# Performance work log

Hardware: AMD Instinct MI355X
Metric: run time of the kernel (lower is better)

Reference implementation:

```python
import jax, jax.numpy as jnp
import numpy as np

KSIZE = 3
KN = (KSIZE - 1) // 2  # 1
TEMP = 50.0


def _extract_patches(x, same_pad):
    """TF tf.image.extract_patches ordering: per location, (dy, dx, channel).
    x: [b,H,W,d] -> [b,h,w,9*d] (h=H,w=W if same_pad else H-2,W-2)."""
    if same_pad:
        x = jnp.pad(x, ((0, 0), (KN, KN), (KN, KN), (0, 0)))
    b, Hp, Wp, d = x.shape
    h, w = Hp - 2 * KN, Wp - 2 * KN
    slices = [x[:, dy:dy + h, dx:dx + w, :]
              for dy in range(KSIZE) for dx in range(KSIZE)]
    return jnp.concatenate(slices, axis=-1)


def setup_inputs() -> dict:
    key = jax.random.key(0)
    k1, k2, k3 = jax.random.split(key, 3)
    b, h, w, dims = 4, 48, 48, 64
    g_in = jax.random.normal(k1, (b, h, w, dims), dtype=jnp.float32)
    # binary inpainting mask (1 = known background, 0 = hole)
    mask = (jax.random.uniform(k2, (b, h, w, 1)) > 0.5).astype(jnp.float32)
    W2 = jax.random.normal(k3, (2 * dims, dims), dtype=jnp.float32) / np.sqrt(2.0 * dims)
    b2 = jnp.zeros((dims,), dtype=jnp.float32)
    return {"g_in": g_in, "mask": mask, "W2": W2, "b2": b2}


def reference(g_in, mask, W2, b2):
    b, h, w, dims = g_in.shape
    c = (h - 2 * KN) * (w - 2 * KN)

    mask_r = mask  # already (h,w,1); broadcasts over dims (== tile)
    bg = g_in * mask_r

    # p1: VALID 3x3 patches of bg -> dynamic kernels, [b, c, 9*dims]
    p1 = _extract_patches(bg, same_pad=False).reshape(b, c, KSIZE * KSIZE * dims)
    # p2: SAME 3x3 patches of g_in, [b, h, w, 9*dims]
    p2 = _extract_patches(g_in, same_pad=True)

    # cross-correlation: conv2d(ft, k1) == per-location dot with each bg patch
    CS = jnp.einsum('byxk,bjk->byxj', p2, p1)              # [b,h,w,c]
    k1d = jnp.sum(p1 * p1, axis=2)                          # [b,c]
    wwd = jnp.sum(p2 * p2, axis=3, keepdims=True)           # [b,h,w,1]
    DS1 = k1d[:, None, None, :] + wwd - 2.0 * CS            # squared distances
    mu = jnp.mean(DS1, axis=3, keepdims=True)
    sd = jnp.std(DS1, axis=3, keepdims=True)                # population std (tf.math.reduce_std)
    DS2 = -jnp.tanh((DS1 - mu) / sd)
    CA = jax.nn.softmax(TEMP * DS2, axis=-1)                # [b,h,w,c]

    # transposed conv aggregation with per-sample kernels k2[b,j,dy,dx,ch]
    k2 = p1.reshape(b, c, KSIZE, KSIZE, dims)
    CA_pad = jnp.pad(CA, ((0, 0), (KN, KN), (KN, KN), (0, 0)))
    acl = jnp.zeros((b, h, w, dims), dtype=g_in.dtype)
    for dy in range(KSIZE):
        for dx in range(KSIZE):
            win = CA_pad[:, 2 * KN - dy:2 * KN - dy + h, 2 * KN - dx:2 * KN - dx + w, :]
            acl = acl + jnp.einsum('byxj,bjd->byxd', win, k2[:, :, dy, dx, :])
    acl = acl / 9.0

    ACL = bg + acl * (1.0 - mask_r)
    con1 = jnp.concatenate([g_in, ACL], axis=3)             # [b,h,w,2*dims]
    return jax.nn.elu(jnp.einsum('byxk,kd->byxd', con1, W2) + b2)
```

## Files before the change

kernel.cpp:

```cpp
#include <hip/hip_runtime.h>
#include <hip/hip_fp16.h>
#include <math.h>

#define BB 4
#define HH 48
#define WW 48
#define DD 64
#define CH 46
#define CWp 46
#define CC (CH*CWp)
#define KK 576
#define HWp (HH*WW)
#define PW 50
#define PP (PW*PW)

#define SLOTW 48
#define NSLOT 2208
#define NGRP 276
#define QW 2304
#define QROWS 2500

typedef __attribute__((ext_vector_type(8))) short short8;
typedef __attribute__((ext_vector_type(8))) _Float16 half8;
typedef __attribute__((ext_vector_type(4))) float float4v;

#define OFFB_GPAD  ((size_t)0)
#define OFFB_BGPAD ((size_t)1280000)
#define OFFB_E     ((size_t)2560000)
#define OFFB_K1D   ((size_t)2596864)
#define OFFB_BGT   ((size_t)2632192)
#define OFFB_Q     ((size_t)3811840)
#define OFFB_S     ((size_t)49891840)
#define OFFB_W     ((size_t)90589696)
#define OFFB_ACL   ((size_t)133057024)

__device__ __forceinline__ ushort f2bf(float x) {
    unsigned u = __float_as_uint(x);
    return (ushort)((u + 0x7FFFu + ((u >> 16) & 1u)) >> 16);
}

__device__ __forceinline__ float waveReduceSum(float x) {
#pragma unroll
    for (int o = 32; o > 0; o >>= 1) x += __shfl_down(x, o, 64);
    return x;
}

__device__ __forceinline__ __half2 u2h2(uint u) {
    union { uint u; __half2 h; } c; c.u = u; return c.h;
}

__device__ __forceinline__ uint cvtpk_bf16(float lo, float hi) {
    uint r;
    asm("v_cvt_pk_bf16_f32 %0, %1, %2" : "=v"(r) : "v"(lo), "v"(hi));
    return r;
}

__device__ __forceinline__ float softexp(float d, float mu, float isd) {
    float z = (d - mu) * isd;
    float E2 = __expf(z + z);
    float r = __builtin_amdgcn_rcpf(E2 + 1.f);
    return __expf(fmaf(100.f, r, -50.f));
}

typedef __attribute__((address_space(3))) void lds_void_t;
typedef __attribute__((address_space(1))) void gmem_void_t;
__device__ __forceinline__ void gld16(const ushort* g, ushort* lds) {
    __builtin_amdgcn_global_load_lds((gmem_void_t*)g, (lds_void_t*)lds, 16, 0, 0);
}

__global__ __launch_bounds__(256) void build_pads(const float* __restrict__ g,
                                                  const float* __restrict__ mask,
                                                  ushort* __restrict__ gpad,
                                                  ushort* __restrict__ bgpad,
                                                  float* __restrict__ e) {
    int w = threadIdx.x >> 6, c = threadIdx.x & 63;
    int q4 = blockIdx.x * 4 + w;
    int b = q4 / PP, q = q4 % PP;
    int yp = q / PW, xp = q % PW;
    size_t o = (size_t)q4 * DD + c;
    if (yp >= 1 && yp <= HH && xp >= 1 && xp <= WW) {
        int pix = (yp - 1) * WW + (xp - 1);
        float gv = g[((size_t)b * HWp + pix) * DD + c];
        float m  = mask[(size_t)b * HWp + pix];
        float bgv = gv * m;
        gpad[o]  = f2bf(gv);
        bgpad[o] = f2bf(bgv);
        float ss = waveReduceSum(bgv * bgv);
        if (c == 0) e[b * HWp + pix] = ss;
    } else {
        gpad[o] = 0;
        bgpad[o] = 0;
    }
}

__global__ __launch_bounds__(256) void build_bgt_k1d(const ushort* __restrict__ bgpad,
                                                     const float* __restrict__ e,
                                                     ushort* __restrict__ bgT,
                                                     float* __restrict__ k1d) {
    int b = blockIdx.y;
    int t = threadIdx.x;
    if (blockIdx.x == 36) {
#pragma unroll 1
        for (int st = t; st < NSLOT; st += 256) {
            int jy = st / SLOTW, jx = st - jy * SLOTW;
            float s = 0.f;
            if (jx < CWp) {
                const float* eb = e + (size_t)b * HWp + jy * WW + jx;
#pragma unroll
                for (int ddy = 0; ddy < 3; ddy++)
#pragma unroll
                    for (int ddx = 0; ddx < 3; ddx++) s += eb[ddy * WW + ddx];
            }
            k1d[(size_t)b * NSLOT + st] = s;
        }
        return;
    }
    __shared__ ushort T[64 * 65];
    int jt = blockIdx.x;
    const ushort* src = bgpad + (size_t)b * PP * DD;
    int lr = t >> 3, c8 = (t & 7) * 8;
#pragma unroll
    for (int pass = 0; pass < 2; pass++) {
        int r = lr + pass * 32;
        int v = jt * 64 + r;
        int vy = v / 48, vx = v - vy * 48;
        uint4 d = *(const uint4*)(src + (size_t)((vy + 1) * PW + (vx + 1)) * DD + c8);
        ushort tmp[8];
        *(uint4*)tmp = d;
#pragma unroll
        for (int u = 0; u < 8; u++) {
            float f = __uint_as_float((uint)tmp[u] << 16);
            __half h = __float2half_rn(f);
            T[r * 65 + c8 + u] = *(ushort*)&h;
        }
    }
    __syncthreads();
#pragma unroll
    for (int pass = 0; pass < 2; pass++) {
        int c = lr + pass * 32;
        int j8 = (t & 7) * 8;
        ushort tmp[8];
#pragma unroll
        for (int u = 0; u < 8; u++) tmp[u] = T[(j8 + u) * 65 + c];
        *(uint4*)(bgT + ((size_t)b * 64 + c) * QW + jt * 64 + j8) = *(const uint4*)tmp;
    }
}

__global__ __launch_bounds__(256) void qgemm(const ushort* __restrict__ gpad,
                                             const ushort* __restrict__ bgpad,
                                             __half* __restrict__ Qout) {
    __shared__ ushort As[2 * 4096];
    __shared__ ushort Bs[2 * 4096];
    int i0 = blockIdx.x;
    int b = (i0 & 7) >> 1;
    int tile = ((i0 >> 3) << 1) | (i0 & 1);
    int ty = tile / 18, tx = tile - ty * 18;
    int m0 = ty * 128, n0 = tx * 128;
    const ushort* Ag = gpad + (size_t)b * PP * DD;
    const ushort* Bg = bgpad + (size_t)b * PP * DD;

    int tid = threadIdx.x;
    int l = tid & 63, w = tid >> 6;
    int quad = l >> 4, l15 = l & 15;
    int sw8 = (l15 >> 1) & 3;
    int wm = (w >> 1) * 64, wn = (w & 1) * 64;
    int rowInC = l >> 2;
    int cSw = (l & 3) ^ ((l >> 3) & 3);

#pragma unroll
    for (int i = 0; i < 2; i++) {
        int rg = w * 2 + i;
        int r = rg * 16 + rowInC;
        int u = m0 + r; if (u > QROWS - 1) u = QROWS - 1;
        int n = n0 + r;
        int vy = n / 48, vx = n - vy * 48;
        int baseA = u * DD + cSw * 8;
        int baseB = ((vy + 1) * PW + (vx + 1)) * DD + cSw * 8;
        gld16(Ag + baseA, As + rg * 512);
        gld16(Bg + baseB, Bs + rg * 512);
        gld16(Ag + baseA + 32, As + 4096 + rg * 512);
        gld16(Bg + baseB + 32, Bs + 4096 + rg * 512);
    }
    float4v acc[4][4];
#pragma unroll
    for (int i = 0; i < 4; i++)
#pragma unroll
        for (int j = 0; j < 4; j++) acc[i][j] = (float4v){0.f, 0.f, 0.f, 0.f};
    __syncthreads();
#pragma unroll
    for (int kb = 0; kb < 2; kb++) {
        const ushort* Ax = As + kb * 4096;
        const ushort* Bx = Bs + kb * 4096;
        short8 af[4], bf[4];
#pragma unroll
        for (int i = 0; i < 4; i++)
            af[i] = *(const short8*)&Ax[(wm + i * 16 + l15) * 32 + ((quad ^ sw8)) * 8];
#pragma unroll
        for (int j = 0; j < 4; j++)
            bf[j] = *(const short8*)&Bx[(wn + j * 16 + l15) * 32 + ((quad ^ sw8)) * 8];
#pragma unroll
        for (int i = 0; i < 4; i++)
#pragma unroll
            for (int j = 0; j < 4; j++)
                acc[i][j] = __builtin_amdgcn_mfma_f32_16x16x32_bf16(af[i], bf[j], acc[i][j], 0, 0, 0);
    }
    __half* C = Qout + (size_t)b * QROWS * QW;
#pragma unroll
    for (int i = 0; i < 4; i++) {
#pragma unroll
        for (int j = 0; j < 4; j++) {
            int n = n0 + wn + j * 16 + l15;
#pragma unroll
            for (int r = 0; r < 4; r++) {
                int m = m0 + wm + i * 16 + quad * 4 + r;
                if (m < QROWS) C[(size_t)m * QW + n] = __float2half(acc[i][j][r]);
            }
        }
    }
}

__global__ __launch_bounds__(320) void qrowsoft3(const __half* __restrict__ Q,
                                                 const float* __restrict__ k1d,
                                                 ushort* __restrict__ CA) {
    __shared__ float red[8][321];
    int i0 = blockIdx.x;
    int b = (i0 & 7) >> 1;
    int sub = ((i0 >> 3) << 1) | (i0 & 1);
    int y = sub / 12, xt = sub - y * 12;
    int x0 = xt * 4;

    int t = threadIdx.x;
    bool act = (t < NGRP);
    int jy = t / 6, jxb = (t - jy * 6) * 8;
    int slot0 = jy * SLOTW + jxb;
    bool vc6 = act && (jxb == 40);

    __half2 acc[4][4];
#pragma unroll
    for (int p = 0; p < 4; p++)
#pragma unroll
        for (int k = 0; k < 4; k++) acc[p][k] = u2h2(0u);

    float k1v[8] = {0.f, 0.f, 0.f, 0.f, 0.f, 0.f, 0.f, 0.f};

    if (act) {
        const float* k1 = k1d + (size_t)b * NSLOT + slot0;
        float4 ka = *(const float4*)k1;
        float4 kb = *(const float4*)(k1 + 4);
        k1v[0] = ka.x; k1v[1] = ka.y; k1v[2] = ka.z; k1v[3] = ka.w;
        k1v[4] = kb.x; k1v[5] = kb.y; k1v[6] = kb.z; k1v[7] = kb.w;

#pragma unroll 1
        for (int dy = 0; dy < 3; dy++) {
            const __half* rp = Q + ((size_t)b * QROWS + (size_t)(y + dy) * PW + x0) * QW
                               + slot0 + dy * 48;
            uint4 W4[6]; uint W1[6];
#pragma unroll
            for (int d = 0; d < 6; d++) {
                const __half* pr = rp + (size_t)d * QW;
                W4[d] = *(const uint4*)pr;
                W1[d] = *(const uint*)(pr + 8);
            }
#pragma unroll
            for (int d = 0; d < 6; d++) {
                uint w0 = W4[d].x, w1 = W4[d].y, w2 = W4[d].z, w3 = W4[d].w, w4 = W1[d];
                if (d < 4) {
                    acc[d][0] = __hadd2(acc[d][0], u2h2(w0));
                    acc[d][1] = __hadd2(acc[d][1], u2h2(w1));
                    acc[d][2] = __hadd2(acc[d][2], u2h2(w2));
                    acc[d][3] = __hadd2(acc[d][3], u2h2(w3));
                }
                if (d >= 1 && d <= 4) {
                    uint s0 = (w0 >> 16) | (w1 << 16);
                    uint s1 = (w1 >> 16) | (w2 << 16);
                    uint s2 = (w2 >> 16) | (w3 << 16);
                    uint s3 = (w3 >> 16) | (w4 << 16);
                    acc[d-1][0] = __hadd2(acc[d-1][0], u2h2(s0));
                    acc[d-1][1] = __hadd2(acc[d-1][1], u2h2(s1));
                    acc[d-1][2] = __hadd2(acc[d-1][2], u2h2(s2));
                    acc[d-1][3] = __hadd2(acc[d-1][3], u2h2(s3));
                }
                if (d >= 2) {
                    acc[d-2][0] = __hadd2(acc[d-2][0], u2h2(w1));
                    acc[d-2][1] = __hadd2(acc[d-2][1], u2h2(w2));
                    acc[d-2][2] = __hadd2(acc[d-2][2], u2h2(w3));
                    acc[d-2][3] = __hadd2(acc[d-2][3], u2h2(w4));
                }
            }
        }
    }

    if (vc6) {
#pragma unroll
        for (int p = 0; p < 4; p++) acc[p][3] = u2h2(0u);
    }

#pragma unroll
    for (int p = 0; p < 4; p++) {
        float s1p = 0.f, s2p = 0.f;
#pragma unroll
        for (int k = 0; k < 4; k++) {
            float2 f = __half22float2(acc[p][k]);
            float d0 = k1v[2*k]   - 2.f * f.x;
            float d1 = k1v[2*k+1] - 2.f * f.y;
            s1p += d0 + d1;
            s2p = fmaf(d0, d0, fmaf(d1, d1, s2p));
        }
        red[p][t] = s1p;
        red[4 + p][t] = s2p;
    }
    __syncthreads();
    if (t < 128) {
        int v = t >> 4, sb = t & 15;
        float s = 0.f;
#pragma unroll
        for (int k = 0; k < 20; k++) s += red[v][sb + 16 * k];
#pragma unroll
        for (int o = 8; o > 0; o >>= 1) s += __shfl_down(s, o, 16);
        if (sb == 0) red[v][320] = s;
    }
    __syncthreads();
    float mu[4], isd[4];
#pragma unroll
    for (int p = 0; p < 4; p++) {
        float m = red[p][320] * (1.f / (float)CC);
        float ex2 = red[4 + p][320] * (1.f / (float)CC);
        mu[p] = m;
        isd[p] = rsqrtf(ex2 - m * m);
    }

    uint eb[4][4];
#pragma unroll
    for (int p = 0; p < 4; p++) {
        float es = 0.f;
#pragma unroll
        for (int k = 0; k < 4; k++) {
            float2 f = __half22float2(acc[p][k]);
            float d0 = k1v[2*k]   - 2.f * f.x;
            float d1 = k1v[2*k+1] - 2.f * f.y;
            if (k == 3 && vc6) { d0 = 1e9f; d1 = 1e9f; }
            float e0 = softexp(d0, mu[p], isd[p]);
            float e1 = softexp(d1, mu[p], isd[p]);
            es += e0 + e1;
            eb[p][k] = cvtpk_bf16(e0, e1);
        }
        red[p][t] = act ? es : 0.f;
    }
    __syncthreads();
    if (t < 64) {
        int v = t >> 4, sb = t & 15;
        float s = 0.f;
#pragma unroll
        for (int k = 0; k < 20; k++) s += red[v][sb + 16 * k];
#pragma unroll
        for (int o = 8; o > 0; o >>= 1) s += __shfl_down(s, o, 16);
        if (sb == 0) red[v][320] = s;
    }
    __syncthreads();

    if (act) {
#pragma unroll
        for (int p = 0; p < 4; p++) {
            float iz = __builtin_amdgcn_rcpf(red[p][320]);
            uint o[4];
#pragma unroll
            for (int k = 0; k < 4; k++) {
                uint wv = eb[p][k];
                float lo = __uint_as_float(wv << 16) * iz;
                float hi = __uint_as_float(wv & 0xffff0000u) * iz;
                __half2 hh = __halves2half2(__float2half_rn(lo), __float2half_rn(hi));
                o[k] = *(uint*)&hh;
            }
            int pix = y * WW + x0 + p;
            ushort* wp = CA + ((size_t)b * HWp + pix) * (size_t)NSLOT + slot0;
            *(uint4*)wp = *(const uint4*)o;
        }
    }
}

__global__ __launch_bounds__(320) void boxsumW(const ushort* __restrict__ CAu,
                                               ushort* __restrict__ Wout) {
    int i0 = blockIdx.x;
    int b = (i0 & 7) >> 1;
    int sub = ((i0 >> 3) << 1) | (i0 & 1);
    int y = sub / 12, xt = sub - y * 12;
    int x0 = xt * 4;

    int t = threadIdx.x;
    if (t >= 288) return;
    int vy = t / 6, vx0 = (t - vy * 6) * 8;

    __half2 acc[4][4];
#pragma unroll
    for (int p = 0; p < 4; p++)
#pragma unroll
        for (int k = 0; k < 4; k++) acc[p][k] = u2h2(0u);

#pragma unroll
    for (int dy = 0; dy < 3; dy++) {
        int yy = y + 1 - dy;
        int jyv = vy - dy;
        if (yy < 0 || yy >= 48 || jyv < 0 || jyv >= 46) continue;
        const ushort* rp = CAu + (size_t)b * HWp * (size_t)NSLOT
                         + (ptrdiff_t)((yy * 48 + x0 - 1) * NSLOT + jyv * 48 + vx0 - 2);
        uint4 W4[6]; uint W1[6];
#pragma unroll
        for (int d = 0; d < 6; d++) {
            int xp = x0 - 1 + d;
            if (xp >= 0 && xp < 48) {
                W4[d] = *(const uint4*)(rp + (size_t)d * NSLOT);
                W1[d] = *(const uint*)(rp + (size_t)d * NSLOT + 8);
            } else {
                W4[d] = make_uint4(0u, 0u, 0u, 0u); W1[d] = 0u;
            }
        }
#pragma unroll
        for (int d = 0; d < 6; d++) {
            uint w0 = W4[d].x, w1 = W4[d].y, w2 = W4[d].z, w3 = W4[d].w, w4 = W1[d];
            if (vx0 == 0) w0 = 0u;
            if (d < 4) {
                acc[d][0] = __hadd2(acc[d][0], u2h2(w0));
                acc[d][1] = __hadd2(acc[d][1], u2h2(w1));
                acc[d][2] = __hadd2(acc[d][2], u2h2(w2));
                acc[d][3] = __hadd2(acc[d][3], u2h2(w3));
            }
            if (d >= 1 && d <= 4) {
                uint s0 = (w0 >> 16) | (w1 << 16);
                uint s1 = (w1 >> 16) | (w2 << 16);
                uint s2 = (w2 >> 16) | (w3 << 16);
                uint s3 = (w3 >> 16) | (w4 << 16);
                acc[d-1][0] = __hadd2(acc[d-1][0], u2h2(s0));
                acc[d-1][1] = __hadd2(acc[d-1][1], u2h2(s1));
                acc[d-1][2] = __hadd2(acc[d-1][2], u2h2(s2));
                acc[d-1][3] = __hadd2(acc[d-1][3], u2h2(s3));
            }
            if (d >= 2) {
                acc[d-2][0] = __hadd2(acc[d-2][0], u2h2(w1));
                acc[d-2][1] = __hadd2(acc[d-2][1], u2h2(w2));
                acc[d-2][2] = __hadd2(acc[d-2][2], u2h2(w3));
                acc[d-2][3] = __hadd2(acc[d-2][3], u2h2(w4));
            }
        }
    }

#pragma unroll
    for (int p = 0; p < 4; p++) {
        uint o[4];
#pragma unroll
        for (int k = 0; k < 4; k++) {
            __half2 h = acc[p][k];
            o[k] = *(uint*)&h;
        }
        size_t row = (size_t)b * HWp + (size_t)(y * 48 + x0 + p);
        *(uint4*)(Wout + row * QW + vy * 48 + vx0) = *(const uint4*)o;
    }
}

__global__ __launch_bounds__(256) void gemm3(const ushort* __restrict__ Wm,
                                             const ushort* __restrict__ bgT,
                                             float* __restrict__ aclp) {
    __shared__ ushort As[2 * 4096];
    __shared__ ushort Bs[2 * 2048];
    int i0 = blockIdx.x;
    int s = i0 & 7;
    int b = (i0 >> 3) & 3;
    int mt = i0 >> 5;
    int m0 = mt * 128;
    int kb = s * 288, ke = kb + 288;
    const ushort* Ab = Wm + ((size_t)b * HWp + m0) * QW;
    const ushort* Bb = bgT + (size_t)b * 64 * QW;

    int tid = threadIdx.x;
    int l = tid & 63, w = tid >> 6;
    int quad = l >> 4, l15 = l & 15;
    int sw8 = (l15 >> 1) & 3;
    int wm = w * 32;
    int rowInC = l >> 2;
    int cSw = (l & 3) ^ ((l >> 3) & 3);

    float4v acc[2][4];
#pragma unroll
    for (int i = 0; i < 2; i++)
#pragma unroll
        for (int j = 0; j < 4; j++) acc[i][j] = (float4v){0.f, 0.f, 0.f, 0.f};

#pragma unroll
    for (int i = 0; i < 2; i++) {
        int rg = w * 2 + i;
        gld16(Ab + (size_t)(rg * 16 + rowInC) * QW + kb + cSw * 8, As + rg * 512);
    }
    gld16(Bb + (size_t)(w * 16 + rowInC) * QW + kb + cSw * 8, Bs + w * 512);

    int buf = 0;
    for (int k0 = kb; k0 < ke; k0 += 32) {
        __syncthreads();
        int nb = buf ^ 1;
        if (k0 + 32 < ke) {
#pragma unroll
            for (int i = 0; i < 2; i++) {
                int rg = w * 2 + i;
                gld16(Ab + (size_t)(rg * 16 + rowInC) * QW + (k0 + 32) + cSw * 8,
                      As + nb * 4096 + rg * 512);
            }
            gld16(Bb + (size_t)(w * 16 + rowInC) * QW + (k0 + 32) + cSw * 8,
                  Bs + nb * 2048 + w * 512);
        }
        const ushort* Ax = As + buf * 4096;
        const ushort* Bx = Bs + buf * 2048;
        half8 af[2], bf[4];
#pragma unroll
        for (int i = 0; i < 2; i++)
            af[i] = *(const half8*)&Ax[(wm + i * 16 + l15) * 32 + ((quad ^ sw8)) * 8];
#pragma unroll
        for (int j = 0; j < 4; j++)
            bf[j] = *(const half8*)&Bx[(j * 16 + l15) * 32 + ((quad ^ sw8)) * 8];
#pragma unroll
        for (int i = 0; i < 2; i++)
#pragma unroll
            for (int j = 0; j < 4; j++)
                acc[i][j] = __builtin_amdgcn_mfma_f32_16x16x32_f16(af[i], bf[j], acc[i][j], 0, 0, 0);
        buf = nb;
    }

    float* C = aclp + ((size_t)s * (BB * HWp) + (size_t)b * HWp) * 64;
#pragma unroll
    for (int i = 0; i < 2; i++)
#pragma unroll
        for (int j = 0; j < 4; j++)
#pragma unroll
            for (int r = 0; r < 4; r++) {
                int m = m0 + wm + i * 16 + quad * 4 + r;
                int n = j * 16 + l15;
                C[(size_t)m * 64 + n] = acc[i][j][r];
            }
}

__global__ __launch_bounds__(256) void final_k2(const float* __restrict__ g,
                                                const float* __restrict__ mask,
                                                const float* __restrict__ aclp,
                                                const float* __restrict__ W2,
                                                const float* __restrict__ b2,
                                                float* __restrict__ out) {
    int w = threadIdx.x >> 6, d = threadIdx.x & 63;
    int pix = blockIdx.x * 4 + w;

    __shared__ float con1[4][128];
    float acl = 0.f;
    const float* ap = aclp + (size_t)pix * 64 + d;
#pragma unroll
    for (int s = 0; s < 8; s++) acl += ap[(size_t)s * (BB * HWp) * 64];

    float m = mask[pix];
    float gv = g[(size_t)pix * DD + d];
    float bgv = gv * m;
    float ACL = bgv + (acl / 9.f) * (1.f - m);
    con1[w][d] = gv;
    con1[w][64 + d] = ACL;
    __syncthreads();
    float accv = b2[d];
#pragma unroll 8
    for (int k = 0; k < 128; k++) accv = fmaf(con1[w][k], W2[k * 64 + d], accv);
    out[(size_t)pix * DD + d] = accv > 0.f ? accv : expm1f(accv);
}

extern "C" void kernel_launch(void* const* d_in, const int* in_sizes, int n_in,
                              void* d_out, int out_size, void* d_ws, size_t ws_size,
                              hipStream_t stream) {
    const float* g    = (const float*)d_in[0];
    const float* mask = (const float*)d_in[1];
    const float* W2   = (const float*)d_in[2];
    const float* b2   = (const float*)d_in[3];
    float* out = (float*)d_out;
    char* ws = (char*)d_ws;

    ushort* gpad  = (ushort*)(ws + OFFB_GPAD);
    ushort* bgpad = (ushort*)(ws + OFFB_BGPAD);
    float*  e     = (float*) (ws + OFFB_E);
    float*  k1d   = (float*) (ws + OFFB_K1D);
    ushort* bgT   = (ushort*)(ws + OFFB_BGT);
    __half* Qbuf  = (__half*)(ws + OFFB_Q);
    ushort* CA    = (ushort*)(ws + OFFB_S);
    ushort* Wbuf  = (ushort*)(ws + OFFB_W);
    float*  aclp  = (float*) (ws + OFFB_ACL);

    build_pads<<<BB * PP / 4, 256, 0, stream>>>(g, mask, gpad, bgpad, e);
    build_bgt_k1d<<<dim3(37, BB), 256, 0, stream>>>(bgpad, e, bgT, k1d);

    qgemm<<<1440, 256, 0, stream>>>(gpad, bgpad, Qbuf);
    qrowsoft3<<<BB * HWp / 4, 320, 0, stream>>>(Qbuf, k1d, CA);

    boxsumW<<<BB * HWp / 4, 320, 0, stream>>>(CA, Wbuf);
    gemm3<<<576, 256, 0, stream>>>(Wbuf, bgT, aclp);

    final_k2<<<BB * HWp / 4, 256, 0, stream>>>(g, mask, aclp, W2, b2, out);
}
```

Baseline: 167.7 us.

## Move dx shifts into GEMM K dimension, splitting box sums between GEMMs and epilogue

Measured after the change: 169.6 us. No clear change (+1.1%).

```diff
diff --git a/kernel.cpp b/kernel.cpp
--- a/kernel.cpp
+++ b/kernel.cpp
@@ -6,10 +6,7 @@
 #define HH 48
 #define WW 48
 #define DD 64
-#define CH 46
-#define CWp 46
-#define CC (CH*CWp)
-#define KK 576
+#define CC 2116
 #define HWp (HH*WW)
 #define PW 50
 #define PP (PW*PW)
@@ -17,6 +14,7 @@
 #define SLOTW 48
 #define NSLOT 2208
 #define NGRP 276
+#define KSPLIT0 1120
 #define QW 2304
 #define QROWS 2500
 
@@ -28,11 +26,11 @@
 #define OFFB_BGPAD ((size_t)1280000)
 #define OFFB_E     ((size_t)2560000)
 #define OFFB_K1D   ((size_t)2596864)
-#define OFFB_BGT   ((size_t)2632192)
-#define OFFB_Q     ((size_t)3811840)
-#define OFFB_S     ((size_t)49891840)
-#define OFFB_W     ((size_t)90589696)
-#define OFFB_ACL   ((size_t)133057024)
+#define OFFB_BGT3  ((size_t)2632192)
+#define OFFB_F     ((size_t)6023680)
+#define OFFB_CA    ((size_t)52103680)
+#define OFFB_CAY   ((size_t)92801536)
+#define OFFB_ACLP  ((size_t)133499392)
 
 __device__ __forceinline__ ushort f2bf(float x) {
     unsigned u = __float_as_uint(x);
@@ -93,18 +91,18 @@
     }
 }
 
-__global__ __launch_bounds__(256) void build_bgt_k1d(const ushort* __restrict__ bgpad,
-                                                     const float* __restrict__ e,
-                                                     ushort* __restrict__ bgT,
-                                                     float* __restrict__ k1d) {
+__global__ __launch_bounds__(256) void build_bgt3_k1d(const ushort* __restrict__ bgpad,
+                                                      const float* __restrict__ e,
+                                                      ushort* __restrict__ bgT3,
+                                                      float* __restrict__ k1d) {
     int b = blockIdx.y;
     int t = threadIdx.x;
-    if (blockIdx.x == 36) {
+    if (blockIdx.x == 35) {
 #pragma unroll 1
         for (int st = t; st < NSLOT; st += 256) {
             int jy = st / SLOTW, jx = st - jy * SLOTW;
             float s = 0.f;
-            if (jx < CWp) {
+            if (jx < 46) {
                 const float* eb = e + (size_t)b * HWp + jy * WW + jx;
 #pragma unroll
                 for (int ddy = 0; ddy < 3; ddy++)
@@ -115,7 +113,7 @@
         }
         return;
     }
-    __shared__ ushort T[64 * 65];
+    __shared__ ushort T[66 * 65];
     int jt = blockIdx.x;
     const ushort* src = bgpad + (size_t)b * PP * DD;
     int lr = t >> 3, c8 = (t & 7) * 8;
@@ -134,21 +132,43 @@
             T[r * 65 + c8 + u] = *(ushort*)&h;
         }
     }
+    if (t < 16) {
+        int r = 64 + (t >> 3);
+        int c8b = (t & 7) * 8;
+        int v = jt * 64 + r;
+        int vy = v / 48, vx = v - vy * 48;
+        uint4 d = *(const uint4*)(src + (size_t)((vy + 1) * PW + (vx + 1)) * DD + c8b);
+        ushort tmp[8];
+        *(uint4*)tmp = d;
+#pragma unroll
+        for (int u = 0; u < 8; u++) {
+            float f = __uint_as_float((uint)tmp[u] << 16);
+            __half h = __float2half_rn(f);
+            T[r * 65 + c8b + u] = *(ushort*)&h;
+        }
+    }
     __syncthreads();
 #pragma unroll
     for (int pass = 0; pass < 2; pass++) {
         int c = lr + pass * 32;
         int j8 = (t & 7) * 8;
-        ushort tmp[8];
-#pragma unroll
-        for (int u = 0; u < 8; u++) tmp[u] = T[(j8 + u) * 65 + c];
-        *(uint4*)(bgT + ((size_t)b * 64 + c) * QW + jt * 64 + j8) = *(const uint4*)tmp;
-    }
-}
-
-__global__ __launch_bounds__(256) void qgemm(const ushort* __restrict__ gpad,
+        int col0 = jt * 64 + j8;
+        if (col0 < NSLOT) {
+#pragma unroll
+            for (int dx = 0; dx < 3; dx++) {
+                ushort tmp[8];
+#pragma unroll
+                for (int u = 0; u < 8; u++) tmp[u] = T[(j8 + u + dx) * 65 + c];
+                *(uint4*)(bgT3 + ((size_t)b * 192 + dx * 64 + c) * NSLOT + col0) =
+                    *(const uint4*)tmp;
+            }
+        }
+    }
+}
+
+__global__ __launch_bounds__(256) void fgemm(const ushort* __restrict__ gpad,
                                              const ushort* __restrict__ bgpad,
-                                             __half* __restrict__ Qout) {
+                                             __half* __restrict__ Fout) {
     __shared__ ushort As[2 * 4096];
     __shared__ ushort Bs[2 * 4096];
     int i0 = blockIdx.x;
@@ -167,6 +187,7 @@
     int rowInC = l >> 2;
     int cSw = (l & 3) ^ ((l >> 3) & 3);
 
+    int baseA[2], baseB[2];
 #pragma unroll
     for (int i = 0; i < 2; i++) {
         int rg = w * 2 + i;
@@ -174,23 +195,37 @@
         int u = m0 + r; if (u > QROWS - 1) u = QROWS - 1;
         int n = n0 + r;
         int vy = n / 48, vx = n - vy * 48;
-        int baseA = u * DD + cSw * 8;
-        int baseB = ((vy + 1) * PW + (vx + 1)) * DD + cSw * 8;
-        gld16(Ag + baseA, As + rg * 512);
-        gld16(Bg + baseB, Bs + rg * 512);
-        gld16(Ag + baseA + 32, As + 4096 + rg * 512);
-        gld16(Bg + baseB + 32, Bs + 4096 + rg * 512);
-    }
+        baseA[i] = u * DD + cSw * 8;
+        baseB[i] = ((vy + 1) * PW + (vx + 1)) * DD + cSw * 8;
+    }
+
     float4v acc[4][4];
 #pragma unroll
     for (int i = 0; i < 4; i++)
 #pragma unroll
         for (int j = 0; j < 4; j++) acc[i][j] = (float4v){0.f, 0.f, 0.f, 0.f};
-    __syncthreads();
-#pragma unroll
-    for (int kb = 0; kb < 2; kb++) {
-        const ushort* Ax = As + kb * 4096;
-        const ushort* Bx = Bs + kb * 4096;
+
+#pragma unroll
+    for (int i = 0; i < 2; i++) {
+        int rg = w * 2 + i;
+        gld16(Ag + baseA[i], As + rg * 512);
+        gld16(Bg + baseB[i], Bs + rg * 512);
+    }
+
+    int buf = 0;
+    for (int k0 = 0; k0 < 192; k0 += 32) {
+        __syncthreads();
+        int nb = buf ^ 1;
+        if (k0 + 32 < 192) {
+#pragma unroll
+            for (int i = 0; i < 2; i++) {
+                int rg = w * 2 + i;
+                gld16(Ag + baseA[i] + (k0 + 32), As + nb * 4096 + rg * 512);
+                gld16(Bg + baseB[i] + (k0 + 32), Bs + nb * 4096 + rg * 512);
+            }
+        }
+        const ushort* Ax = As + buf * 4096;
+        const ushort* Bx = Bs + buf * 4096;
         short8 af[4], bf[4];
 #pragma unroll
         for (int i = 0; i < 4; i++)
@@ -203,8 +238,10 @@
 #pragma unroll
             for (int j = 0; j < 4; j++)
                 acc[i][j] = __builtin_amdgcn_mfma_f32_16x16x32_bf16(af[i], bf[j], acc[i][j], 0, 0, 0);
-    }
-    __half* C = Qout + (size_t)b * QROWS * QW;
+        buf = nb;
+    }
+
+    __half* C = Fout + (size_t)b * QROWS * QW;
 #pragma unroll
     for (int i = 0; i < 4; i++) {
 #pragma unroll
@@ -219,7 +256,7 @@
     }
 }
 
-__global__ __launch_bounds__(320) void qrowsoft3(const __half* __restrict__ Q,
+__global__ __launch_bounds__(320) void qrowsoft4(const __half* __restrict__ F,
                                                  const float* __restrict__ k1d,
                                                  ushort* __restrict__ CA) {
     __shared__ float red[8][321];
@@ -250,42 +287,17 @@
         k1v[0] = ka.x; k1v[1] = ka.y; k1v[2] = ka.z; k1v[3] = ka.w;
         k1v[4] = kb.x; k1v[5] = kb.y; k1v[6] = kb.z; k1v[7] = kb.w;
 
-#pragma unroll 1
+#pragma unroll
         for (int dy = 0; dy < 3; dy++) {
-            const __half* rp = Q + ((size_t)b * QROWS + (size_t)(y + dy) * PW + x0) * QW
-                               + slot0 + dy * 48;
-            uint4 W4[6]; uint W1[6];
-#pragma unroll
-            for (int d = 0; d < 6; d++) {
-                const __half* pr = rp + (size_t)d * QW;
-                W4[d] = *(const uint4*)pr;
-                W1[d] = *(const uint*)(pr + 8);
-            }
-#pragma unroll
-            for (int d = 0; d < 6; d++) {
-                uint w0 = W4[d].x, w1 = W4[d].y, w2 = W4[d].z, w3 = W4[d].w, w4 = W1[d];
-                if (d < 4) {
-                    acc[d][0] = __hadd2(acc[d][0], u2h2(w0));
-                    acc[d][1] = __hadd2(acc[d][1], u2h2(w1));
-                    acc[d][2] = __hadd2(acc[d][2], u2h2(w2));
-                    acc[d][3] = __hadd2(acc[d][3], u2h2(w3));
-                }
-                if (d >= 1 && d <= 4) {
-                    uint s0 = (w0 >> 16) | (w1 << 16);
-                    uint s1 = (w1 >> 16) | (w2 << 16);
-                    uint s2 = (w2 >> 16) | (w3 << 16);
-                    uint s3 = (w3 >> 16) | (w4 << 16);
-                    acc[d-1][0] = __hadd2(acc[d-1][0], u2h2(s0));
-                    acc[d-1][1] = __hadd2(acc[d-1][1], u2h2(s1));
-                    acc[d-1][2] = __hadd2(acc[d-1][2], u2h2(s2));
-                    acc[d-1][3] = __hadd2(acc[d-1][3], u2h2(s3));
-                }
-                if (d >= 2) {
-                    acc[d-2][0] = __hadd2(acc[d-2][0], u2h2(w1));
-                    acc[d-2][1] = __hadd2(acc[d-2][1], u2h2(w2));
-                    acc[d-2][2] = __hadd2(acc[d-2][2], u2h2(w3));
-                    acc[d-2][3] = __hadd2(acc[d-2][3], u2h2(w4));
-                }
+            const __half* R = F + ((size_t)b * QROWS + (size_t)(y + dy) * PW + x0) * QW
+                            + slot0 + dy * 48;
+#pragma unroll
+            for (int p = 0; p < 4; p++) {
+                uint4 v4 = *(const uint4*)(R + (size_t)p * QW);
+                acc[p][0] = __hadd2(acc[p][0], u2h2(v4.x));
+                acc[p][1] = __hadd2(acc[p][1], u2h2(v4.y));
+                acc[p][2] = __hadd2(acc[p][2], u2h2(v4.z));
+                acc[p][3] = __hadd2(acc[p][3], u2h2(v4.w));
             }
         }
     }
@@ -378,8 +390,8 @@
     }
 }
 
-__global__ __launch_bounds__(320) void boxsumW(const ushort* __restrict__ CAu,
-                                               ushort* __restrict__ Wout) {
+__global__ __launch_bounds__(320) void cay_k(const ushort* __restrict__ CAu,
+                                             ushort* __restrict__ CAy) {
     int i0 = blockIdx.x;
     int b = (i0 & 7) >> 1;
     int sub = ((i0 >> 3) << 1) | (i0 & 1);
@@ -387,8 +399,9 @@
     int x0 = xt * 4;
 
     int t = threadIdx.x;
-    if (t >= 288) return;
-    int vy = t / 6, vx0 = (t - vy * 6) * 8;
+    if (t >= NGRP) return;
+    int jy = t / 6, jxb = (t - jy * 6) * 8;
+    int slot0 = jy * SLOTW + jxb;
 
     __half2 acc[4][4];
 #pragma unroll
@@ -399,47 +412,17 @@
 #pragma unroll
     for (int dy = 0; dy < 3; dy++) {
         int yy = y + 1 - dy;
-        int jyv = vy - dy;
-        if (yy < 0 || yy >= 48 || jyv < 0 || jyv >= 46) continue;
-        const ushort* rp = CAu + (size_t)b * HWp * (size_t)NSLOT
-                         + (ptrdiff_t)((yy * 48 + x0 - 1) * NSLOT + jyv * 48 + vx0 - 2);
-        uint4 W4[6]; uint W1[6];
-#pragma unroll
-        for (int d = 0; d < 6; d++) {
-            int xp = x0 - 1 + d;
-            if (xp >= 0 && xp < 48) {
-                W4[d] = *(const uint4*)(rp + (size_t)d * NSLOT);
-                W1[d] = *(const uint*)(rp + (size_t)d * NSLOT + 8);
-            } else {
-                W4[d] = make_uint4(0u, 0u, 0u, 0u); W1[d] = 0u;
-            }
-        }
-#pragma unroll
-        for (int d = 0; d < 6; d++) {
-            uint w0 = W4[d].x, w1 = W4[d].y, w2 = W4[d].z, w3 = W4[d].w, w4 = W1[d];
-            if (vx0 == 0) w0 = 0u;
-            if (d < 4) {
-                acc[d][0] = __hadd2(acc[d][0], u2h2(w0));
-                acc[d][1] = __hadd2(acc[d][1], u2h2(w1));
-                acc[d][2] = __hadd2(acc[d][2], u2h2(w2));
-                acc[d][3] = __hadd2(acc[d][3], u2h2(w3));
-            }
-            if (d >= 1 && d <= 4) {
-                uint s0 = (w0 >> 16) | (w1 << 16);
-                uint s1 = (w1 >> 16) | (w2 << 16);
-                uint s2 = (w2 >> 16) | (w3 << 16);
-                uint s3 = (w3 >> 16) | (w4 << 16);
-                acc[d-1][0] = __hadd2(acc[d-1][0], u2h2(s0));
-                acc[d-1][1] = __hadd2(acc[d-1][1], u2h2(s1));
-                acc[d-1][2] = __hadd2(acc[d-1][2], u2h2(s2));
-                acc[d-1][3] = __hadd2(acc[d-1][3], u2h2(s3));
-            }
-            if (d >= 2) {
-                acc[d-2][0] = __hadd2(acc[d-2][0], u2h2(w1));
-                acc[d-2][1] = __hadd2(acc[d-2][1], u2h2(w2));
-                acc[d-2][2] = __hadd2(acc[d-2][2], u2h2(w3));
-                acc[d-2][3] = __hadd2(acc[d-2][3], u2h2(w4));
-            }
+        if (yy < 0 || yy >= 48) continue;
+        if (jy < dy) continue;
+        const ushort* rp = CAu + ((size_t)b * HWp + yy * 48 + x0) * (size_t)NSLOT
+                         + slot0 - 48 * dy;
+#pragma unroll
+        for (int p = 0; p < 4; p++) {
+            uint4 v4 = *(const uint4*)(rp + (size_t)p * NSLOT);
+            acc[p][0] = __hadd2(acc[p][0], u2h2(v4.x));
+            acc[p][1] = __hadd2(acc[p][1], u2h2(v4.y));
+            acc[p][2] = __hadd2(acc[p][2], u2h2(v4.z));
+            acc[p][3] = __hadd2(acc[p][3], u2h2(v4.w));
         }
     }
 
@@ -451,24 +434,26 @@
             __half2 h = acc[p][k];
             o[k] = *(uint*)&h;
         }
-        size_t row = (size_t)b * HWp + (size_t)(y * 48 + x0 + p);
-        *(uint4*)(Wout + row * QW + vy * 48 + vx0) = *(const uint4*)o;
-    }
-}
-
-__global__ __launch_bounds__(256) void gemm3(const ushort* __restrict__ Wm,
-                                             const ushort* __restrict__ bgT,
+        *(uint4*)(CAy + ((size_t)b * HWp + y * 48 + x0 + p) * (size_t)NSLOT + slot0) =
+            *(const uint4*)o;
+    }
+}
+
+__global__ __launch_bounds__(256) void gemm4(const ushort* __restrict__ Am,
+                                             const ushort* __restrict__ Bm,
                                              float* __restrict__ aclp) {
     __shared__ ushort As[2 * 4096];
     __shared__ ushort Bs[2 * 2048];
     int i0 = blockIdx.x;
-    int s = i0 & 7;
-    int b = (i0 >> 3) & 3;
-    int mt = i0 >> 5;
-    int m0 = mt * 128;
-    int kb = s * 288, ke = kb + 288;
-    const ushort* Ab = Wm + ((size_t)b * HWp + m0) * QW;
-    const ushort* Bb = bgT + (size_t)b * 64 * QW;
+    int z = i0 & 7;
+    int b = z >> 1, s = z & 1;
+    int tile = i0 >> 3;
+    int ty = tile / 3, tx = tile - ty * 3;
+    int m0 = ty * 128, n0 = tx * 64;
+    int kb = s ? KSPLIT0 : 0;
+    int ke = s ? NSLOT : KSPLIT0;
+    const ushort* Ab = Am + ((size_t)b * HWp + m0) * (size_t)NSLOT;
+    const ushort* Bb = Bm + ((size_t)b * 192 + n0) * (size_t)NSLOT;
 
     int tid = threadIdx.x;
     int l = tid & 63, w = tid >> 6;
@@ -487,9 +472,9 @@
 #pragma unroll
     for (int i = 0; i < 2; i++) {
         int rg = w * 2 + i;
-        gld16(Ab + (size_t)(rg * 16 + rowInC) * QW + kb + cSw * 8, As + rg * 512);
-    }
-    gld16(Bb + (size_t)(w * 16 + rowInC) * QW + kb + cSw * 8, Bs + w * 512);
+        gld16(Ab + (size_t)(rg * 16 + rowInC) * NSLOT + kb + cSw * 8, As + rg * 512);
+    }
+    gld16(Bb + (size_t)(w * 16 + rowInC) * NSLOT + kb + cSw * 8, Bs + w * 512);
 
     int buf = 0;
     for (int k0 = kb; k0 < ke; k0 += 32) {
@@ -499,10 +484,10 @@
 #pragma unroll
             for (int i = 0; i < 2; i++) {
                 int rg = w * 2 + i;
-                gld16(Ab + (size_t)(rg * 16 + rowInC) * QW + (k0 + 32) + cSw * 8,
+                gld16(Ab + (size_t)(rg * 16 + rowInC) * NSLOT + (k0 + 32) + cSw * 8,
                       As + nb * 4096 + rg * 512);
             }
-            gld16(Bb + (size_t)(w * 16 + rowInC) * QW + (k0 + 32) + cSw * 8,
+            gld16(Bb + (size_t)(w * 16 + rowInC) * NSLOT + (k0 + 32) + cSw * 8,
                   Bs + nb * 2048 + w * 512);
         }
         const ushort* Ax = As + buf * 4096;
@@ -522,7 +507,7 @@
         buf = nb;
     }
 
-    float* C = aclp + ((size_t)s * (BB * HWp) + (size_t)b * HWp) * 64;
+    float* C = aclp + ((size_t)s * (BB * HWp) + (size_t)b * HWp) * 192;
 #pragma unroll
     for (int i = 0; i < 2; i++)
 #pragma unroll
@@ -530,12 +515,12 @@
 #pragma unroll
             for (int r = 0; r < 4; r++) {
                 int m = m0 + wm + i * 16 + quad * 4 + r;
-                int n = j * 16 + l15;
-                C[(size_t)m * 64 + n] = acc[i][j][r];
-            }
-}
-
-__global__ __launch_bounds__(256) void final_k2(const float* __restrict__ g,
+                int n = n0 + j * 16 + l15;
+                C[(size_t)m * 192 + n] = acc[i][j][r];
+            }
+}
+
+__global__ __launch_bounds__(256) void final_k3(const float* __restrict__ g,
                                                 const float* __restrict__ mask,
                                                 const float* __restrict__ aclp,
                                                 const float* __restrict__ W2,
@@ -543,12 +528,19 @@
                                                 float* __restrict__ out) {
     int w = threadIdx.x >> 6, d = threadIdx.x & 63;
     int pix = blockIdx.x * 4 + w;
+    int b = pix / HWp, yx = pix % HWp;
+    int y = yx / WW, x = yx % WW;
 
     __shared__ float con1[4][128];
     float acl = 0.f;
-    const float* ap = aclp + (size_t)pix * 64 + d;
-#pragma unroll
-    for (int s = 0; s < 8; s++) acl += ap[(size_t)s * (BB * HWp) * 64];
+#pragma unroll
+    for (int dx = 0; dx < 3; dx++) {
+        int xs = x + 1 - dx;
+        if (xs >= 0 && xs < WW) {
+            size_t off = ((size_t)b * HWp + y * WW + xs) * 192 + dx * 64 + d;
+            acl += aclp[off] + aclp[off + (size_t)BB * HWp * 192];
+        }
+    }
 
     float m = mask[pix];
     float gv = g[(size_t)pix * DD + d];
@@ -577,20 +569,20 @@
     ushort* bgpad = (ushort*)(ws + OFFB_BGPAD);
     float*  e     = (float*) (ws + OFFB_E);
     float*  k1d   = (float*) (ws + OFFB_K1D);
-    ushort* bgT   = (ushort*)(ws + OFFB_BGT);
-    __half* Qbuf  = (__half*)(ws + OFFB_Q);
-    ushort* CA    = (ushort*)(ws + OFFB_S);
-    ushort* Wbuf  = (ushort*)(ws + OFFB_W);
-    float*  aclp  = (float*) (ws + OFFB_ACL);
+    ushort* bgT3  = (ushort*)(ws + OFFB_BGT3);
+    __half* Fbuf  = (__half*)(ws + OFFB_F);
+    ushort* CA    = (ushort*)(ws + OFFB_CA);
+    ushort* CAy   = (ushort*)(ws + OFFB_CAY);
+    float*  aclp  = (float*) (ws + OFFB_ACLP);
 
     build_pads<<<BB * PP / 4, 256, 0, stream>>>(g, mask, gpad, bgpad, e);
-    build_bgt_k1d<<<dim3(37, BB), 256, 0, stream>>>(bgpad, e, bgT, k1d);
-
-    qgemm<<<1440, 256, 0, stream>>>(gpad, bgpad, Qbuf);
-    qrowsoft3<<<BB * HWp / 4, 320, 0, stream>>>(Qbuf, k1d, CA);
-
-    boxsumW<<<BB * HWp / 4, 320, 0, stream>>>(CA, Wbuf);
-    gemm3<<<576, 256, 0, stream>>>(Wbuf, bgT, aclp);
-
-    final_k2<<<BB * HWp / 4, 256, 0, stream>>>(g, mask, aclp, W2, b2, out);
-}
+    build_bgt3_k1d<<<dim3(36, BB), 256, 0, stream>>>(bgpad, e, bgT3, k1d);
+
+    fgemm<<<1440, 256, 0, stream>>>(gpad, bgpad, Fbuf);
+    qrowsoft4<<<BB * HWp / 4, 320, 0, stream>>>(Fbuf, k1d, CA);
+
+    cay_k<<<BB * HWp / 4, 320, 0, stream>>>(CA, CAy);
+    gemm4<<<432, 256, 0, stream>>>(CAy, bgT3, aclp);
+
+    final_k3<<<BB * HWp / 4, 256, 0, stream>>>(g, mask, aclp, W2, b2, out);
+}
```
